# Kernel tuning notes

Hardware: AMD Instinct MI355X
Metric: run time of the kernel (lower is better)

Reference implementation:

```python
import jax, jax.numpy as jnp
import numpy as np
import math

H = 8  # num_heads

def setup_inputs() -> dict:
    key = jax.random.key(0)
    ks = jax.random.split(key, 12)
    B, N, M, k = 2, 8192, 8192, 32
    dq, dk, dv = 256, 256, 256
    s = 1.0 / math.sqrt(dq)
    inp = {
        'Q': jax.random.normal(ks[0], (B, N, dq), dtype=jnp.float32),
        'K': jax.random.normal(ks[1], (B, M, dk), dtype=jnp.float32),
        'neighbours': jax.random.randint(ks[2], (B, N, k), 0, M),
        'Wq': jax.random.normal(ks[3], (dq, dv), dtype=jnp.float32) * s,
        'bq': jnp.zeros((dv,), dtype=jnp.float32),
        'Wk': jax.random.normal(ks[4], (dk, dv), dtype=jnp.float32) * s,
        'bk': jnp.zeros((dv,), dtype=jnp.float32),
        'Wv': jax.random.normal(ks[5], (dk, dv), dtype=jnp.float32) * s,
        'bv': jnp.zeros((dv,), dtype=jnp.float32),
        'Wo': jax.random.normal(ks[6], (dv, dv), dtype=jnp.float32) * (1.0 / math.sqrt(dv)),
        'bo': jnp.zeros((dv,), dtype=jnp.float32),
    }
    return inp

def reference(Q, K, neighbours, Wq, bq, Wk, bk, Wv, bv, Wo, bo):
    B, N, _ = Q.shape
    dv = Wq.shape[1]
    ds = dv // H
    # project and split heads (contiguous channel chunks == reshape)
    Qh = (Q @ Wq + bq).reshape(B, N, H, ds)            # [B,N,H,ds]
    Kh = (K @ Wk + bk).reshape(B, -1, H, ds)           # [B,M,H,ds]
    Vh = (K @ Wv + bv).reshape(B, -1, H, ds)           # [B,M,H,ds]
    # gather per-node kNN neighbour keys/values: [B,N,k,H,ds]
    gather = jax.vmap(lambda x, idx: x[idx])
    Kn = gather(Kh, neighbours)
    Vn = gather(Vh, neighbours)
    # scale uses full latent size (faithful to original), not head dim
    scale = 1.0 / math.sqrt(dv)
    E = jnp.einsum('bnhd,bnkhd->bnhk', Qh, Kn) * scale  # [B,N,H,k]
    A = jax.nn.softmax(E, axis=-1)
    AV = jnp.einsum('bnhk,bnkhd->bnhd', A, Vn).reshape(B, N, dv)
    return AV @ Wo + bo
```

## Files before the change

### kernel.cpp

```cpp
#include <hip/hip_runtime.h>
#include <stdint.h>

typedef unsigned short u16;
typedef __attribute__((ext_vector_type(8))) short short8;
typedef __attribute__((ext_vector_type(4))) float f32x4;

__device__ __forceinline__ float bf2f(u16 u) {
    union { unsigned int i; float f; } v;
    v.i = ((unsigned int)u) << 16;
    return v.f;
}
__device__ __forceinline__ u16 f2bf(float f) {
    union { float f; unsigned int i; } v; v.f = f;
    unsigned int b = v.i;
    return (u16)((b + 0x7FFFu + ((b >> 16) & 1u)) >> 16);
}

typedef const __attribute__((address_space(1))) void* as1cv;
typedef __attribute__((address_space(3))) void* as3v;
__device__ __forceinline__ void gload16(const void* g, void* l) {
    __builtin_amdgcn_global_load_lds((as1cv)g, (as3v)l, 16, 0, 0);
}

__global__ __launch_bounds__(256) void prep(
    const float* __restrict__ Q, const float* __restrict__ K,
    const float* __restrict__ Wq, const float* __restrict__ Wk,
    const float* __restrict__ Wv, const float* __restrict__ Wo,
    u16* __restrict__ Qb, u16* __restrict__ Kb,
    u16* __restrict__ Tq, u16* __restrict__ Tk,
    u16* __restrict__ Tv, u16* __restrict__ To)
{
    __shared__ u16 ts[64][65];
    int bi = blockIdx.x;
    int t = threadIdx.x;
    if (bi < 4096) {
        const float* src = (bi < 2048) ? Q : K;
        u16* dst = (bi < 2048) ? Qb : Kb;
        int blk = bi & 2047;
        size_t i = ((size_t)blk * 256 + t) * 8;
        float4 a = *reinterpret_cast<const float4*>(src + i);
        float4 b = *reinterpret_cast<const float4*>(src + i + 4);
        u16 o[8] = {f2bf(a.x), f2bf(a.y), f2bf(a.z), f2bf(a.w),
                    f2bf(b.x), f2bf(b.y), f2bf(b.z), f2bf(b.w)};
        *reinterpret_cast<uint4*>(dst + i) = *reinterpret_cast<const uint4*>(o);
        return;
    }
    int wi = bi - 4096;
    int wsel = wi >> 4;
    const float* W = wsel == 0 ? Wq : wsel == 1 ? Wk : wsel == 2 ? Wv : Wo;
    u16*        T  = wsel == 0 ? Tq : wsel == 1 ? Tk : wsel == 2 ? Tv : To;
    int k0 = ((wi >> 2) & 3) * 64, n0 = (wi & 3) * 64;
    int r = t >> 2, cq = (t & 3) * 16;
    const float4* src = reinterpret_cast<const float4*>(W + (k0 + r) * 256 + n0 + cq);
    for (int u = 0; u < 4; ++u) {
        float4 v = src[u];
        int c = cq + u * 4;
        ts[r][c + 0] = f2bf(v.x); ts[r][c + 1] = f2bf(v.y);
        ts[r][c + 2] = f2bf(v.z); ts[r][c + 3] = f2bf(v.w);
    }
    __syncthreads();
    u16* dst = T + (n0 + r) * 256 + k0 + cq;
    for (int u = 0; u < 16; ++u) dst[u] = ts[cq + u][r];
}

template <bool F32OUT>
__device__ __forceinline__ void gemm_core(
    const u16* __restrict__ Ab, const u16* __restrict__ Wt,
    const float* __restrict__ bias, void* __restrict__ Cv,
    int row0, int col0)
{
    __shared__ u16 As[128 * 64];
    __shared__ u16 Bs[128 * 64];

    int t = threadIdx.x;
    int lane = t & 63, w = t >> 6;
    int wr = (w >> 1) * 64, wc = (w & 1) * 64;
    int qd = lane >> 4, md = lane & 15;

    int srow = w * 32 + (lane >> 3);
    int scol = (lane & 7) * 8;

    f32x4 acc[4][4] = {};

    for (int kt = 0; kt < 256; kt += 64) {
#pragma unroll
        for (int u = 0; u < 4; ++u) {
            int r = srow + u * 8;
            gload16(Ab + (size_t)(row0 + r) * 256 + kt + scol,
                    (char*)As + (w * 4 + u) * 1024);
            gload16(Wt + (size_t)(col0 + r) * 256 + kt + scol,
                    (char*)Bs + (w * 4 + u) * 1024);
        }
        __syncthreads();
#pragma unroll
        for (int ks = 0; ks < 64; ks += 32) {
            short8 af[4], bf[4];
#pragma unroll
            for (int i = 0; i < 4; ++i)
                af[i] = *reinterpret_cast<const short8*>(
                    &As[(wr + i * 16 + md) * 64 + ks + qd * 8]);
#pragma unroll
            for (int j = 0; j < 4; ++j)
                bf[j] = *reinterpret_cast<const short8*>(
                    &Bs[(wc + j * 16 + md) * 64 + ks + qd * 8]);
#pragma unroll
            for (int i = 0; i < 4; ++i)
#pragma unroll
                for (int j = 0; j < 4; ++j)
                    acc[i][j] = __builtin_amdgcn_mfma_f32_16x16x32_bf16(
                        af[i], bf[j], acc[i][j], 0, 0, 0);
        }
        __syncthreads();
    }

#pragma unroll
    for (int i = 0; i < 4; ++i)
#pragma unroll
        for (int j = 0; j < 4; ++j) {
            int col = col0 + wc + j * 16 + md;
            float b = bias[col];
#pragma unroll
            for (int r = 0; r < 4; ++r) {
                int row = row0 + wr + i * 16 + qd * 4 + r;
                if (F32OUT)
                    ((float*)Cv)[(size_t)row * 256 + col] = acc[i][j][r] + b;
                else
                    ((u16*)Cv)[(size_t)row * 256 + col] = f2bf(acc[i][j][r] + b);
            }
        }
}

__global__ __launch_bounds__(256) void gemm_proj(
    const u16* __restrict__ Qb, const u16* __restrict__ Kb,
    const u16* __restrict__ Wtq, const u16* __restrict__ Wtk, const u16* __restrict__ Wtv,
    const float* __restrict__ bq, const float* __restrict__ bk, const float* __restrict__ bv,
    u16* __restrict__ Qh, u16* __restrict__ Kh, u16* __restrict__ Vh)
{
    int z = blockIdx.z;
    const u16*   A    = (z == 0) ? Qb  : Kb;
    const u16*   Wt   = (z == 0) ? Wtq : (z == 1) ? Wtk : Wtv;
    const float* bias = (z == 0) ? bq  : (z == 1) ? bk  : bv;
    u16*         C    = (z == 0) ? Qh  : (z == 1) ? Kh  : Vh;
    gemm_core<false>(A, Wt, bias, C, blockIdx.x * 128, blockIdx.y * 128);
}

__global__ __launch_bounds__(256) void gemm_out(
    const u16* __restrict__ A, const u16* __restrict__ Wt,
    const float* __restrict__ bias, float* __restrict__ Cout)
{
    gemm_core<true>(A, Wt, bias, Cout, blockIdx.x * 128, blockIdx.y * 128);
}

__global__ __launch_bounds__(256) void attn(
    const u16* __restrict__ Qh, const u16* __restrict__ Kh, const u16* __restrict__ Vh,
    const int* __restrict__ nbr, u16* __restrict__ AVb)
{
    __shared__ float qs[2][256];
    __shared__ float as_[2][256];
    __shared__ int jb[2][32];

    int t = threadIdx.x;
    int row0 = blockIdx.x * 2;
    int b = row0 >> 13;

    {
        int r = t >> 7, c = (t & 127) * 2;
        unsigned int v = *reinterpret_cast<const unsigned int*>(
            Qh + (size_t)(row0 + r) * 256 + c);
        union { unsigned int i; float f; } lo, hi;
        lo.i = v << 16; hi.i = v & 0xffff0000u;
        qs[r][c] = lo.f; qs[r][c + 1] = hi.f;
    }
    if (t < 64) {
        int r = t >> 5, j = t & 31;
        int ji = nbr[(size_t)(row0 + r) * 32 + j];
        jb[r][j] = ((b << 13) + ji) << 9;
    }
    __syncthreads();

    int h = t >> 5, j = t & 31;
#pragma unroll
    for (int r = 0; r < 2; ++r) {
        const char* kp = (const char*)Kh + jb[r][j] + h * 64;
        uint4 kw[4];
        kw[0] = *reinterpret_cast<const uint4*>(kp);
        kw[1] = *reinterpret_cast<const uint4*>(kp + 16);
        kw[2] = *reinterpret_cast<const uint4*>(kp + 32);
        kw[3] = *reinterpret_cast<const uint4*>(kp + 48);
        const float* q = &qs[r][h * 32];
        float e = 0.f;
#pragma unroll
        for (int cq4 = 0; cq4 < 4; ++cq4) {
            unsigned int wds[4] = {kw[cq4].x, kw[cq4].y, kw[cq4].z, kw[cq4].w};
#pragma unroll
            for (int u = 0; u < 4; ++u) {
                union { unsigned int i; float f; } lo, hi;
                lo.i = wds[u] << 16; hi.i = wds[u] & 0xffff0000u;
                e += q[cq4 * 8 + u * 2] * lo.f + q[cq4 * 8 + u * 2 + 1] * hi.f;
            }
        }
        e *= 0.0625f;
        float m = e;
        for (int off = 16; off; off >>= 1) m = fmaxf(m, __shfl_xor(m, off, 32));
        float p = __expf(e - m);
        float s = p;
        for (int off = 16; off; off >>= 1) s += __shfl_xor(s, off, 32);
        as_[r][t] = p / s;
    }
    __syncthreads();

    {
        int r = t >> 7, c = t & 127, hh = c >> 4;
        const float* aw = &as_[r][hh * 32];
        float a0 = 0.f, a1 = 0.f;
#pragma unroll
        for (int jj = 0; jj < 32; ++jj) {
            unsigned int v = *reinterpret_cast<const unsigned int*>(
                (const char*)Vh + jb[r][jj] + c * 4);
            union { unsigned int i; float f; } lo, hi;
            lo.i = v << 16; hi.i = v & 0xffff0000u;
            float wgt = aw[jj];
            a0 += wgt * lo.f; a1 += wgt * hi.f;
        }
        u16 o[2] = {f2bf(a0), f2bf(a1)};
        *reinterpret_cast<unsigned int*>(AVb + (size_t)(row0 + r) * 256 + c * 2) =
            *reinterpret_cast<const unsigned int*>(o);
    }
}

extern "C" void kernel_launch(void* const* d_in, const int* in_sizes, int n_in,
                              void* d_out, int out_size, void* d_ws, size_t ws_size,
                              hipStream_t stream) {
    const float* Q   = (const float*)d_in[0];
    const float* K   = (const float*)d_in[1];
    const int*   nbr = (const int*)d_in[2];
    const float* Wq  = (const float*)d_in[3];
    const float* bq  = (const float*)d_in[4];
    const float* Wk  = (const float*)d_in[5];
    const float* bk  = (const float*)d_in[6];
    const float* Wv  = (const float*)d_in[7];
    const float* bv  = (const float*)d_in[8];
    const float* Wo  = (const float*)d_in[9];
    const float* bo  = (const float*)d_in[10];
    float* out = (float*)d_out;

    char* ws = (char*)d_ws;
    size_t off = 0;
    auto alloc = [&](size_t bytes) -> void* {
        void* p = ws + off;
        off += (bytes + 255) & ~(size_t)255;
        return p;
    };
    const size_t MN = 16384;
    u16* Wtq = (u16*)alloc(256 * 256 * 2);
    u16* Wtk = (u16*)alloc(256 * 256 * 2);
    u16* Wtv = (u16*)alloc(256 * 256 * 2);
    u16* Wto = (u16*)alloc(256 * 256 * 2);
    u16* Qb  = (u16*)alloc(MN * 256 * 2);
    u16* Kb  = (u16*)alloc(MN * 256 * 2);
    u16* Qh  = (u16*)alloc(MN * 256 * 2);
    u16* Kh  = (u16*)alloc(MN * 256 * 2);
    u16* Vh  = (u16*)alloc(MN * 256 * 2);
    u16* AVb = (u16*)alloc(MN * 256 * 2);

    prep<<<dim3(4160), 256, 0, stream>>>(Q, K, Wq, Wk, Wv, Wo,
                                         Qb, Kb, Wtq, Wtk, Wtv, Wto);
    gemm_proj<<<dim3(128, 2, 3), 256, 0, stream>>>(Qb, Kb, Wtq, Wtk, Wtv,
                                                   bq, bk, bv, Qh, Kh, Vh);
    attn<<<dim3(8192), 256, 0, stream>>>(Qh, Kh, Vh, nbr, AVb);
    gemm_out<<<dim3(128, 2, 1), 256, 0, stream>>>(AVb, Wto, bo, out);
}
```

Before: 168.2 us.

## Fuse fp32-to-bf16 input conversion into thin-tile projection GEMMs

Result: slower. 181.4 us (+7.9%).

```diff
diff --git a/kernel.cpp b/kernel.cpp
--- a/kernel.cpp
+++ b/kernel.cpp
@@ -5,51 +5,23 @@
 typedef __attribute__((ext_vector_type(8))) short short8;
 typedef __attribute__((ext_vector_type(4))) float f32x4;
 
-__device__ __forceinline__ float bf2f(u16 u) {
-    union { unsigned int i; float f; } v;
-    v.i = ((unsigned int)u) << 16;
-    return v.f;
-}
 __device__ __forceinline__ u16 f2bf(float f) {
     union { float f; unsigned int i; } v; v.f = f;
     unsigned int b = v.i;
     return (u16)((b + 0x7FFFu + ((b >> 16) & 1u)) >> 16);
 }
 
-typedef const __attribute__((address_space(1))) void* as1cv;
-typedef __attribute__((address_space(3))) void* as3v;
-__device__ __forceinline__ void gload16(const void* g, void* l) {
-    __builtin_amdgcn_global_load_lds((as1cv)g, (as3v)l, 16, 0, 0);
-}
-
-__global__ __launch_bounds__(256) void prep(
-    const float* __restrict__ Q, const float* __restrict__ K,
-    const float* __restrict__ Wq, const float* __restrict__ Wk,
-    const float* __restrict__ Wv, const float* __restrict__ Wo,
-    u16* __restrict__ Qb, u16* __restrict__ Kb,
-    u16* __restrict__ Tq, u16* __restrict__ Tk,
-    u16* __restrict__ Tv, u16* __restrict__ To)
-{
+__global__ __launch_bounds__(256) void wprep(
+    const float* __restrict__ W0, const float* __restrict__ W1,
+    const float* __restrict__ W2, const float* __restrict__ W3,
+    u16* __restrict__ T0, u16* __restrict__ T1,
+    u16* __restrict__ T2, u16* __restrict__ T3)
+{
+    const float* W = blockIdx.z == 0 ? W0 : blockIdx.z == 1 ? W1 : blockIdx.z == 2 ? W2 : W3;
+    u16*        T  = blockIdx.z == 0 ? T0 : blockIdx.z == 1 ? T1 : blockIdx.z == 2 ? T2 : T3;
     __shared__ u16 ts[64][65];
-    int bi = blockIdx.x;
+    int k0 = blockIdx.x * 64, n0 = blockIdx.y * 64;
     int t = threadIdx.x;
-    if (bi < 4096) {
-        const float* src = (bi < 2048) ? Q : K;
-        u16* dst = (bi < 2048) ? Qb : Kb;
-        int blk = bi & 2047;
-        size_t i = ((size_t)blk * 256 + t) * 8;
-        float4 a = *reinterpret_cast<const float4*>(src + i);
-        float4 b = *reinterpret_cast<const float4*>(src + i + 4);
-        u16 o[8] = {f2bf(a.x), f2bf(a.y), f2bf(a.z), f2bf(a.w),
-                    f2bf(b.x), f2bf(b.y), f2bf(b.z), f2bf(b.w)};
-        *reinterpret_cast<uint4*>(dst + i) = *reinterpret_cast<const uint4*>(o);
-        return;
-    }
-    int wi = bi - 4096;
-    int wsel = wi >> 4;
-    const float* W = wsel == 0 ? Wq : wsel == 1 ? Wk : wsel == 2 ? Wv : Wo;
-    u16*        T  = wsel == 0 ? Tq : wsel == 1 ? Tk : wsel == 2 ? Tv : To;
-    int k0 = ((wi >> 2) & 3) * 64, n0 = (wi & 3) * 64;
     int r = t >> 2, cq = (t & 3) * 16;
     const float4* src = reinterpret_cast<const float4*>(W + (k0 + r) * 256 + n0 + cq);
     for (int u = 0; u < 4; ++u) {
@@ -63,61 +35,72 @@
     for (int u = 0; u < 16; ++u) dst[u] = ts[cq + u][r];
 }
 
-template <bool F32OUT>
-__device__ __forceinline__ void gemm_core(
-    const u16* __restrict__ Ab, const u16* __restrict__ Wt,
+#define KPAD 264
+
+template <bool A_F32, bool F32OUT>
+__device__ __forceinline__ void gemm_thin(
+    const void* __restrict__ Aptr, const u16* __restrict__ Wt,
     const float* __restrict__ bias, void* __restrict__ Cv,
     int row0, int col0)
 {
-    __shared__ u16 As[128 * 64];
-    __shared__ u16 Bs[128 * 64];
+    __shared__ __align__(16) u16 Bs[64 * KPAD];
 
     int t = threadIdx.x;
     int lane = t & 63, w = t >> 6;
-    int wr = (w >> 1) * 64, wc = (w & 1) * 64;
     int qd = lane >> 4, md = lane & 15;
 
-    int srow = w * 32 + (lane >> 3);
-    int scol = (lane & 7) * 8;
-
-    f32x4 acc[4][4] = {};
-
-    for (int kt = 0; kt < 256; kt += 64) {
-#pragma unroll
-        for (int u = 0; u < 4; ++u) {
-            int r = srow + u * 8;
-            gload16(Ab + (size_t)(row0 + r) * 256 + kt + scol,
-                    (char*)As + (w * 4 + u) * 1024);
-            gload16(Wt + (size_t)(col0 + r) * 256 + kt + scol,
-                    (char*)Bs + (w * 4 + u) * 1024);
-        }
-        __syncthreads();
-#pragma unroll
-        for (int ks = 0; ks < 64; ks += 32) {
-            short8 af[4], bf[4];
-#pragma unroll
-            for (int i = 0; i < 4; ++i)
+    {
+        int cj = t >> 2, c0 = t & 3;
+        const uint4* src = reinterpret_cast<const uint4*>(Wt + (size_t)(col0 + cj) * 256);
+        uint4* dstrow = reinterpret_cast<uint4*>(&Bs[cj * KPAD]);
+#pragma unroll
+        for (int s = 0; s < 8; ++s) {
+            int c = c0 + s * 4;
+            dstrow[c] = src[c];
+        }
+    }
+    __syncthreads();
+
+    int wr = w * 32;
+    f32x4 acc[2][4] = {};
+
+#pragma unroll
+    for (int kk = 0; kk < 8; ++kk) {
+        int k0 = kk * 32 + qd * 8;
+        short8 af[2];
+#pragma unroll
+        for (int i = 0; i < 2; ++i) {
+            size_t row = (size_t)(row0 + wr + i * 16 + md);
+            if (A_F32) {
+                const float* ap = (const float*)Aptr + row * 256 + k0;
+                float4 a0 = *reinterpret_cast<const float4*>(ap);
+                float4 a1 = *reinterpret_cast<const float4*>(ap + 4);
+                u16 o[8] = {f2bf(a0.x), f2bf(a0.y), f2bf(a0.z), f2bf(a0.w),
+                            f2bf(a1.x), f2bf(a1.y), f2bf(a1.z), f2bf(a1.w)};
+                af[i] = *reinterpret_cast<const short8*>(o);
+            } else {
                 af[i] = *reinterpret_cast<const short8*>(
-                    &As[(wr + i * 16 + md) * 64 + ks + qd * 8]);
+                    (const u16*)Aptr + row * 256 + k0);
+            }
+        }
+        short8 bf[4];
+#pragma unroll
+        for (int j = 0; j < 4; ++j)
+            bf[j] = *reinterpret_cast<const short8*>(
+                &Bs[(j * 16 + md) * KPAD + k0]);
+#pragma unroll
+        for (int i = 0; i < 2; ++i)
 #pragma unroll
             for (int j = 0; j < 4; ++j)
-                bf[j] = *reinterpret_cast<const short8*>(
-                    &Bs[(wc + j * 16 + md) * 64 + ks + qd * 8]);
-#pragma unroll
-            for (int i = 0; i < 4; ++i)
-#pragma unroll
-                for (int j = 0; j < 4; ++j)
-                    acc[i][j] = __builtin_amdgcn_mfma_f32_16x16x32_bf16(
-                        af[i], bf[j], acc[i][j], 0, 0, 0);
-        }
-        __syncthreads();
-    }
-
-#pragma unroll
-    for (int i = 0; i < 4; ++i)
+                acc[i][j] = __builtin_amdgcn_mfma_f32_16x16x32_bf16(
+                    af[i], bf[j], acc[i][j], 0, 0, 0);
+    }
+
+#pragma unroll
+    for (int i = 0; i < 2; ++i)
 #pragma unroll
         for (int j = 0; j < 4; ++j) {
-            int col = col0 + wc + j * 16 + md;
+            int col = col0 + j * 16 + md;
             float b = bias[col];
 #pragma unroll
             for (int r = 0; r < 4; ++r) {
@@ -131,24 +114,24 @@
 }
 
 __global__ __launch_bounds__(256) void gemm_proj(
-    const u16* __restrict__ Qb, const u16* __restrict__ Kb,
+    const float* __restrict__ Q, const float* __restrict__ K,
     const u16* __restrict__ Wtq, const u16* __restrict__ Wtk, const u16* __restrict__ Wtv,
     const float* __restrict__ bq, const float* __restrict__ bk, const float* __restrict__ bv,
     u16* __restrict__ Qh, u16* __restrict__ Kh, u16* __restrict__ Vh)
 {
     int z = blockIdx.z;
-    const u16*   A    = (z == 0) ? Qb  : Kb;
+    const float* A    = (z == 0) ? Q   : K;
     const u16*   Wt   = (z == 0) ? Wtq : (z == 1) ? Wtk : Wtv;
     const float* bias = (z == 0) ? bq  : (z == 1) ? bk  : bv;
     u16*         C    = (z == 0) ? Qh  : (z == 1) ? Kh  : Vh;
-    gemm_core<false>(A, Wt, bias, C, blockIdx.x * 128, blockIdx.y * 128);
+    gemm_thin<true, false>(A, Wt, bias, C, blockIdx.x * 128, blockIdx.y * 64);
 }
 
 __global__ __launch_bounds__(256) void gemm_out(
     const u16* __restrict__ A, const u16* __restrict__ Wt,
     const float* __restrict__ bias, float* __restrict__ Cout)
 {
-    gemm_core<true>(A, Wt, bias, Cout, blockIdx.x * 128, blockIdx.y * 128);
+    gemm_thin<false, true>(A, Wt, bias, Cout, blockIdx.x * 128, blockIdx.y * 64);
 }
 
 __global__ __launch_bounds__(256) void attn(
@@ -256,17 +239,14 @@
     u16* Wtk = (u16*)alloc(256 * 256 * 2);
     u16* Wtv = (u16*)alloc(256 * 256 * 2);
     u16* Wto = (u16*)alloc(256 * 256 * 2);
-    u16* Qb  = (u16*)alloc(MN * 256 * 2);
-    u16* Kb  = (u16*)alloc(MN * 256 * 2);
     u16* Qh  = (u16*)alloc(MN * 256 * 2);
     u16* Kh  = (u16*)alloc(MN * 256 * 2);
     u16* Vh  = (u16*)alloc(MN * 256 * 2);
     u16* AVb = (u16*)alloc(MN * 256 * 2);
 
-    prep<<<dim3(4160), 256, 0, stream>>>(Q, K, Wq, Wk, Wv, Wo,
-                                         Qb, Kb, Wtq, Wtk, Wtv, Wto);
-    gemm_proj<<<dim3(128, 2, 3), 256, 0, stream>>>(Qb, Kb, Wtq, Wtk, Wtv,
+    wprep<<<dim3(4, 4, 4), 256, 0, stream>>>(Wq, Wk, Wv, Wo, Wtq, Wtk, Wtv, Wto);
+    gemm_proj<<<dim3(128, 4, 3), 256, 0, stream>>>(Q, K, Wtq, Wtk, Wtv,
                                                    bq, bk, bv, Qh, Kh, Vh);
     attn<<<dim3(8192), 256, 0, stream>>>(Qh, Kh, Vh, nbr, AVb);
-    gemm_out<<<dim3(128, 2, 1), 256, 0, stream>>>(AVb, Wto, bo, out);
-}
+    gemm_out<<<dim3(128, 4), 256, 0, stream>>>(AVb, Wto, bo, out);
+}
```
